# Performance work log

Hardware: AMD Instinct MI355X
Metric: run time of the kernel (lower is better)

Reference implementation:

```python
import jax, jax.numpy as jnp
import numpy as np

EPS = 1e-6
LN3 = 1.0986122886681098  # ternary_softmax uses base-3 exponentials: 3**x / sum(3**x)
ROPE_BASE = 10000.0


def exact_rmsnorm(x, g):
    # ExactRMSNorm: x / sqrt(mean(x^2) + eps) * g
    ms = jnp.mean(jnp.square(x), axis=-1, keepdims=True)
    return x * jax.lax.rsqrt(ms + EPS) * g


def ternary_rope(t):
    # Rotary embedding whose cos/sin tables are quantized to {-1, 0, +1}
    # (round() of cos/sin in [-1,1] yields exactly the ternary set).
    S, D = t.shape[-2], t.shape[-1]
    half = D // 2
    inv_freq = 1.0 / (ROPE_BASE ** (jnp.arange(half, dtype=jnp.float32) / half))
    ang = jnp.arange(S, dtype=jnp.float32)[:, None] * inv_freq[None, :]  # [S, half]
    cos = jnp.round(jnp.cos(ang))
    sin = jnp.round(jnp.sin(ang))
    cos = jnp.concatenate([cos, cos], axis=-1)  # [S, D]
    sin = jnp.concatenate([sin, sin], axis=-1)
    rot = jnp.concatenate([-t[..., half:], t[..., :half]], axis=-1)
    return t * cos + rot * sin


def ternary_softmax(x, axis=-1):
    # softmax in base 3: 3**x / sum(3**x) == softmax(x * ln 3)
    return jax.nn.softmax(x * LN3, axis=axis)


def setup_inputs() -> dict:
    key = jax.random.key(0)
    ks = jax.random.split(key, 6)
    B, S, D = 4, 4096, 1024
    x = jax.random.normal(ks[0], (B, S, D), dtype=jnp.float32)
    g_norm = jnp.ones((D,), dtype=jnp.float32)
    w_qkv = jax.random.normal(ks[1], (D, 3 * D), dtype=jnp.float32) * 0.02
    b_qkv = jnp.zeros((3 * D,), dtype=jnp.float32)
    w_proj = jax.random.normal(ks[2], (D, D), dtype=jnp.float32) * 0.02
    b_proj = jnp.zeros((D,), dtype=jnp.float32)
    return {"x": x, "g_norm": g_norm, "w_qkv": w_qkv, "b_qkv": b_qkv,
            "w_proj": w_proj, "b_proj": b_proj}


def reference(x, g_norm, w_qkv, b_qkv, w_proj, b_proj):
    D = x.shape[-1]
    scale = 1.0 / jnp.sqrt(jnp.float32(D))
    residual = x
    h = exact_rmsnorm(x, g_norm)
    qkv = h @ w_qkv + b_qkv  # [B, S, 3D]
    q, k, v = jnp.split(qkv, 3, axis=-1)
    q = ternary_rope(q)
    k = ternary_rope(k)
    scores = jnp.einsum("bsd,btd->bst", q, k) * scale  # [B, S, S]
    attn = ternary_softmax(scores, axis=-1)
    o = jnp.einsum("bst,btd->bsd", attn, v)
    return o @ w_proj + b_proj + residual
```

## Files before the change

### kernel.cpp

```cpp
#include <hip/hip_runtime.h>
#include <hip/hip_fp8.h>
#include <stdint.h>

#define DEVI __device__ __forceinline__

typedef unsigned short u16;
typedef uint8_t u8;
typedef __attribute__((ext_vector_type(8))) __bf16 bf16x8;
typedef __attribute__((ext_vector_type(4))) float f32x4;
typedef __attribute__((ext_vector_type(4))) int i32x4;
typedef __attribute__((ext_vector_type(8))) int i32x8;

DEVI float b2f(u16 u) { union { unsigned int i; float f; } v; v.i = ((unsigned int)u) << 16; return v.f; }
DEVI u16 f2b(float f) {
  union { float f; unsigned int i; } v; v.f = f;
  unsigned int r = v.i + 0x7fffu + ((v.i >> 16) & 1u);
  return (u16)(r >> 16);
}
DEVI u8 f2f8(float f) { __hip_fp8_e4m3 t(f); return t.__x; }

DEVI void gld_lds16(const void* g, void* l) {
  __builtin_amdgcn_global_load_lds((const __attribute__((address_space(1))) unsigned int*)g,
                                   (__attribute__((address_space(3))) unsigned int*)l, 16, 0, 0);
}

DEVI i32x8 ld32(const u8* p0, const u8* p1) {
  i32x4 lo = *(const i32x4*)p0;
  i32x4 hi = *(const i32x4*)p1;
  return __builtin_shufflevector(lo, hi, 0, 1, 2, 3, 4, 5, 6, 7);
}


__global__ __launch_bounds__(256) void k_rmsnorm(const float* __restrict__ x,
                                                 const float* __restrict__ g,
                                                 u8* __restrict__ h) {
  const int row = blockIdx.x;
  const int t = threadIdx.x;
  const float4 v = ((const float4*)(x + (size_t)row * 1024))[t];
  float ss = v.x * v.x + v.y * v.y + v.z * v.z + v.w * v.w;
  for (int off = 32; off > 0; off >>= 1) ss += __shfl_down(ss, off);
  __shared__ float red[4];
  if ((t & 63) == 0) red[t >> 6] = ss;
  __syncthreads();
  const float tot = red[0] + red[1] + red[2] + red[3];
  const float sc = rsqrtf(tot * (1.0f / 1024.0f) + 1e-6f);
  const float4 gv = ((const float4*)g)[t];
  uchar4 o;
  o.x = f2f8(v.x * sc * gv.x); o.y = f2f8(v.y * sc * gv.y);
  o.z = f2f8(v.z * sc * gv.z); o.w = f2f8(v.w * sc * gv.w);
  *(uchar4*)(h + (size_t)row * 1024 + t * 4) = o;
}

__global__ __launch_bounds__(256) void k_transpose_cast(const float* __restrict__ src,
                                                        int rows, int cols,
                                                        u16* __restrict__ dst) {
  __shared__ float tile[32][33];
  const int c0 = blockIdx.x * 32, r0 = blockIdx.y * 32;
  const int tx = threadIdx.x, ty = threadIdx.y;
  for (int i = 0; i < 32; i += 8)
    tile[ty + i][tx] = src[(size_t)(r0 + ty + i) * cols + c0 + tx];
  __syncthreads();
  for (int i = 0; i < 32; i += 8)
    dst[(size_t)(c0 + ty + i) * rows + r0 + tx] = f2b(tile[tx][ty + i]);
}

__global__ __launch_bounds__(256) void k_transpose_cast_f8(const float* __restrict__ src,
                                                           int rows, int cols,
                                                           u8* __restrict__ dst) {
  __shared__ float tile[32][33];
  const int c0 = blockIdx.x * 32, r0 = blockIdx.y * 32;
  const int tx = threadIdx.x, ty = threadIdx.y;
  for (int i = 0; i < 32; i += 8)
    tile[ty + i][tx] = src[(size_t)(r0 + ty + i) * cols + c0 + tx];
  __syncthreads();
  for (int i = 0; i < 32; i += 8)
    dst[(size_t)(c0 + ty + i) * rows + r0 + tx] = f2f8(tile[tx][ty + i] * 32.0f);
}

__global__ __launch_bounds__(256) void k_rope_cast(const u16* __restrict__ q16, const u16* __restrict__ k16,
                                                   u8* __restrict__ q8, u8* __restrict__ k8) {
  const int row = blockIdx.x;
  const int pos = row & 4095;
  const int t = threadIdx.x;
  const int j0 = t * 2;
  float c[2], s[2];
#pragma unroll
  for (int u = 0; u < 2; u++) {
    const float e = (float)(j0 + u) * (1.0f / 512.0f);
    const float invf = exp2f(-13.287712379549449f * e);
    const float ang = (float)pos * invf;
    c[u] = rintf(cosf(ang));
    s[u] = rintf(sinf(ang));
  }
  const u16* qr = q16 + (size_t)row * 1024;
  const u16* kr = k16 + (size_t)row * 1024;
  u8* qo = q8 + (size_t)row * 1024;
  u8* ko = k8 + (size_t)row * 1024;
  const ushort2 qa = *(const ushort2*)(qr + j0), qb = *(const ushort2*)(qr + j0 + 512);
  const ushort2 ka = *(const ushort2*)(kr + j0), kb = *(const ushort2*)(kr + j0 + 512);
  uchar2 o;
  o.x = f2f8(b2f(qa.x) * c[0] - b2f(qb.x) * s[0]);
  o.y = f2f8(b2f(qa.y) * c[1] - b2f(qb.y) * s[1]);
  *(uchar2*)(qo + j0) = o;
  o.x = f2f8(b2f(qb.x) * c[0] + b2f(qa.x) * s[0]);
  o.y = f2f8(b2f(qb.y) * c[1] + b2f(qa.y) * s[1]);
  *(uchar2*)(qo + j0 + 512) = o;
  o.x = f2f8(b2f(ka.x) * c[0] - b2f(kb.x) * s[0]);
  o.y = f2f8(b2f(ka.y) * c[1] - b2f(kb.y) * s[1]);
  *(uchar2*)(ko + j0) = o;
  o.x = f2f8(b2f(kb.x) * c[0] + b2f(ka.x) * s[0]);
  o.y = f2f8(b2f(kb.y) * c[1] + b2f(ka.y) * s[1]);
  *(uchar2*)(ko + j0 + 512) = o;
}

__global__ __launch_bounds__(256) void k_vt(const u16* __restrict__ v, u8* __restrict__ vt) {
  __shared__ u16 tile[32][33];
  const int b = blockIdx.z;
  const int s0 = blockIdx.x * 32, d0 = blockIdx.y * 32;
  const int tx = threadIdx.x, ty = threadIdx.y;
  for (int i = 0; i < 32; i += 8)
    tile[ty + i][tx] = v[(size_t)(b * 4096 + s0 + ty + i) * 1024 + d0 + tx];
  __syncthreads();
  for (int i = 0; i < 32; i += 8)
    vt[(size_t)(b * 1024 + d0 + ty + i) * 4096 + s0 + tx] = f2f8(b2f(tile[tx][ty + i]));
}

DEVI void gemm_tile(const u16* __restrict__ A, int lda,
                    const u16* __restrict__ B, int ldb,
                    int K, int m0, int n0,
                    u16* As, u16* Bs, f32x4 acc[4][4]) {
  const int t = threadIdx.x;
  const int sr = t >> 2;
  const int sc = (t & 3) * 8;
  const u16* Ag0 = A + (size_t)(m0 + sr) * lda + sc;
  const u16* Ag1 = A + (size_t)(m0 + 64 + sr) * lda + sc;
  const u16* Bg0 = B + (size_t)(n0 + sr) * ldb + sc;
  const u16* Bg1 = B + (size_t)(n0 + 64 + sr) * ldb + sc;
  u16* Asw0 = As + t * 8;
  u16* Asw1 = As + 2048 + t * 8;
  u16* Bsw0 = Bs + t * 8;
  u16* Bsw1 = Bs + 2048 + t * 8;

  const int lane = t & 63, qd = lane >> 4, l16 = lane & 15;
  const int wave = t >> 6;
  const int wm = (wave >> 1) * 64, wn = (wave & 1) * 64;
  const u16* Ard = As + (size_t)(wm + l16) * 32 + qd * 8;
  const u16* Brd = Bs + (size_t)(wn + l16) * 32 + qd * 8;

  for (int k0 = 0; k0 < K; k0 += 32) {
    gld_lds16(Ag0 + k0, Asw0);
    gld_lds16(Ag1 + k0, Asw1);
    gld_lds16(Bg0 + k0, Bsw0);
    gld_lds16(Bg1 + k0, Bsw1);
    __builtin_amdgcn_s_waitcnt(0);
    __syncthreads();
    bf16x8 af[4], bfv[4];
#pragma unroll
    for (int i = 0; i < 4; i++) af[i] = *(const bf16x8*)(Ard + i * 16 * 32);
#pragma unroll
    for (int j = 0; j < 4; j++) bfv[j] = *(const bf16x8*)(Brd + j * 16 * 32);
#pragma unroll
    for (int i = 0; i < 4; i++)
#pragma unroll
      for (int j = 0; j < 4; j++)
        acc[i][j] = __builtin_amdgcn_mfma_f32_16x16x32_bf16(af[i], bfv[j], acc[i][j], 0, 0, 0);
    __syncthreads();
  }
}

DEVI void gemm_tile_mx(const u8* __restrict__ A, int lda,
                       const u8* __restrict__ B, int ldb,
                       int K, int m0, int n0,
                       u8* As, u8* Bs, f32x4 acc[4][4], int sB) {
  const int t = threadIdx.x;
  const int sr = t >> 3;
  const int sc = ((t & 7) ^ (sr & 7)) << 4;
  const u8* Agb = A + (size_t)(m0 + sr) * lda + sc;
  const u8* Bgb = B + (size_t)(n0 + sr) * ldb + sc;
  u8* Asw = As + t * 16;
  u8* Bsw = Bs + t * 16;

  const int lane = t & 63, qd = lane >> 4, l16 = lane & 15;
  const int wave = t >> 6;
  const int wm = (wave >> 1) * 64, wn = (wave & 1) * 64;
  const int key = l16 & 7;
  const int c0 = ((qd << 1) ^ key) << 4;
  const u8* Ar0 = As + (size_t)(wm + l16) * 128 + c0;
  const u8* Ar1 = As + (size_t)(wm + l16) * 128 + (c0 ^ 16);
  const u8* Br0 = Bs + (size_t)(wn + l16) * 128 + c0;
  const u8* Br1 = Bs + (size_t)(wn + l16) * 128 + (c0 ^ 16);

  for (int k0 = 0; k0 < K; k0 += 128) {
#pragma unroll
    for (int l = 0; l < 4; l++) {
      gld_lds16(Agb + k0 + (size_t)l * 32 * lda, Asw + l * 4096);
      gld_lds16(Bgb + k0 + (size_t)l * 32 * ldb, Bsw + l * 4096);
    }
    __builtin_amdgcn_s_waitcnt(0);
    __syncthreads();
    i32x8 a[4], b[4];
#pragma unroll
    for (int i = 0; i < 4; i++) a[i] = ld32(Ar0 + i * 2048, Ar1 + i * 2048);
#pragma unroll
    for (int j = 0; j < 4; j++) b[j] = ld32(Br0 + j * 2048, Br1 + j * 2048);
#pragma unroll
    for (int i = 0; i < 4; i++)
#pragma unroll
      for (int j = 0; j < 4; j++)
        acc[i][j] = __builtin_amdgcn_mfma_scale_f32_16x16x128_f8f6f4(
            a[i], b[j], acc[i][j], 0 , 0 ,
            0, 0x7f7f7f7f, 0, sB);
    __syncthreads();
  }
}

#define ACC_INIT()                                               \
  f32x4 acc[4][4];                                               \
  _Pragma("unroll") for (int i = 0; i < 4; i++)                  \
      _Pragma("unroll") for (int j = 0; j < 4; j++)              \
          acc[i][j] = f32x4{0.f, 0.f, 0.f, 0.f};

#define GEMM_EPI_IDX()                                           \
  const int t = threadIdx.x, lane = t & 63, qd = lane >> 4,      \
            l16 = lane & 15, wave = t >> 6;                      \
  const int wm = (wave >> 1) * 64, wn = (wave & 1) * 64;         \
  (void)t;


__global__ __launch_bounds__(256) void k_gemm_qkv(const u8* __restrict__ A, const u8* __restrict__ Bt,
                                                  const float* __restrict__ bias,
                                                  u16* __restrict__ q16, u16* __restrict__ k16,
                                                  u16* __restrict__ v16) {
  __shared__ alignas(16) u8 As[16384], Bs[16384];
  ACC_INIT();
  const int m0 = blockIdx.y * 128, n0 = blockIdx.x * 128;
  gemm_tile_mx(A, 1024, Bt, 1024, 1024, m0, n0, As, Bs, acc, 0x7a7a7a7a);
  GEMM_EPI_IDX();
  const int sec = n0 >> 10;
  u16* dst = (sec == 0) ? q16 : (sec == 1) ? k16 : v16;
  const int nb0 = n0 & 1023;
#pragma unroll
  for (int i = 0; i < 4; i++) {
    const int mb = m0 + wm + i * 16 + qd * 4;
#pragma unroll
    for (int j = 0; j < 4; j++) {
      const int col = n0 + wn + j * 16 + l16;
      const float bv = bias[col];
      const int dcol = nb0 + wn + j * 16 + l16;
#pragma unroll
      for (int r = 0; r < 4; r++)
        dst[(size_t)(mb + r) * 1024 + dcol] = f2b(acc[i][j][r] + bv);
    }
  }
}

__global__ __launch_bounds__(256) void k_gemm_scores(const u8* __restrict__ q, const u8* __restrict__ kk,
                                                     u8* __restrict__ P, float* __restrict__ ls) {
  __shared__ alignas(16) u8 As[16384], Bs[16384];
  ACC_INIT();
  const int b = blockIdx.z;
  const u8* A = q + (size_t)b * 4096 * 1024;
  const u8* Bt = kk + (size_t)b * 4096 * 1024;
  const int bid = blockIdx.y * 32 + blockIdx.x;
  const int xcd = bid & 7, idx = bid >> 3;
  const int m0 = ((xcd >> 2) * 16 + (idx & 15)) * 128;
  const int n0 = ((xcd & 3) * 8 + (idx >> 4)) * 128;
  gemm_tile_mx(A, 1024, Bt, 1024, 1024, m0, n0, As, Bs, acc, 0x7f7f7f7f);
  GEMM_EPI_IDX();
  const float C3 = 0.04953007814753613f;
  const size_t Pb = (size_t)b * 4096 * 4096;
  f32x4 rowp[4];
#pragma unroll
  for (int i = 0; i < 4; i++) rowp[i] = f32x4{0.f, 0.f, 0.f, 0.f};
#pragma unroll
  for (int i = 0; i < 4; i++) {
    const int mb = m0 + wm + i * 16 + qd * 4;
#pragma unroll
    for (int j = 0; j < 4; j++) {
      const int col = n0 + wn + j * 16 + l16;
#pragma unroll
      for (int r = 0; r < 4; r++) {
        const float pv = exp2f(acc[i][j][r] * C3);
        P[Pb + (size_t)(mb + r) * 4096 + col] = f2f8(pv);
        rowp[i][r] += pv;
      }
    }
  }
#pragma unroll
  for (int m = 1; m < 16; m <<= 1)
#pragma unroll
    for (int i = 0; i < 4; i++) {
      rowp[i].x += __shfl_xor(rowp[i].x, m);
      rowp[i].y += __shfl_xor(rowp[i].y, m);
      rowp[i].z += __shfl_xor(rowp[i].z, m);
      rowp[i].w += __shfl_xor(rowp[i].w, m);
    }
  if (l16 == 0) {
#pragma unroll
    for (int i = 0; i < 4; i++) {
      const int mb = m0 + wm + i * 16 + qd * 4;
#pragma unroll
      for (int r = 0; r < 4; r++)
        atomicAdd(ls + (size_t)b * 4096 + mb + r, rowp[i][r]);
    }
  }
}

__global__ __launch_bounds__(256) void k_gemm_pv(const u8* __restrict__ P, const u8* __restrict__ vt,
                                                 const float* __restrict__ ls, u16* __restrict__ o) {
  __shared__ alignas(16) u8 As[16384], Bs[16384];
  ACC_INIT();
  const int b = blockIdx.z;
  const u8* A = P + (size_t)b * 4096 * 4096;
  const u8* Bt = vt + (size_t)b * 1024 * 4096;
  const int bid = blockIdx.y * 8 + blockIdx.x;
  const int xcd = bid & 7, idx = bid >> 3;
  const int m0 = ((xcd >> 1) * 8 + (idx & 7)) * 128;
  const int n0 = ((xcd & 1) * 4 + (idx >> 3)) * 128;
  gemm_tile_mx(A, 4096, Bt, 4096, 4096, m0, n0, As, Bs, acc, 0x7f7f7f7f);
  GEMM_EPI_IDX();
#pragma unroll
  for (int i = 0; i < 4; i++) {
    const int mb = m0 + wm + i * 16 + qd * 4;
    f32x4 inv;
#pragma unroll
    for (int r = 0; r < 4; r++) inv[r] = 1.0f / ls[(size_t)b * 4096 + mb + r];
#pragma unroll
    for (int j = 0; j < 4; j++) {
      const int col = n0 + wn + j * 16 + l16;
#pragma unroll
      for (int r = 0; r < 4; r++)
        o[(size_t)(b * 4096 + mb + r) * 1024 + col] = f2b(acc[i][j][r] * inv[r]);
    }
  }
}

__global__ __launch_bounds__(256) void k_gemm_proj(const u16* __restrict__ A, const u16* __restrict__ Bt,
                                                   const float* __restrict__ bias, const float* __restrict__ x,
                                                   float* __restrict__ out) {
  __shared__ alignas(16) u16 As[4096], Bs[4096];
  ACC_INIT();
  const int m0 = blockIdx.y * 128, n0 = blockIdx.x * 128;
  gemm_tile(A, 1024, Bt, 1024, 1024, m0, n0, As, Bs, acc);
  GEMM_EPI_IDX();
#pragma unroll
  for (int i = 0; i < 4; i++) {
    const int mb = m0 + wm + i * 16 + qd * 4;
#pragma unroll
    for (int j = 0; j < 4; j++) {
      const int col = n0 + wn + j * 16 + l16;
      const float bv = bias[col];
#pragma unroll
      for (int r = 0; r < 4; r++) {
        const size_t idxo = (size_t)(mb + r) * 1024 + col;
        out[idxo] = acc[i][j][r] + bv + x[idxo];
      }
    }
  }
}

extern "C" void kernel_launch(void* const* d_in, const int* in_sizes, int n_in,
                              void* d_out, int out_size, void* d_ws, size_t ws_size,
                              hipStream_t stream) {
  const float* x     = (const float*)d_in[0];
  const float* g     = (const float*)d_in[1];
  const float* wqkv  = (const float*)d_in[2];
  const float* bqkv  = (const float*)d_in[3];
  const float* wproj = (const float*)d_in[4];
  const float* bproj = (const float*)d_in[5];
  float* out = (float*)d_out;

  char* wsp = (char*)d_ws;
  size_t off = 0;
  auto take = [&](size_t bytes) -> void* {
    off = (off + 255) & ~(size_t)255;
    void* r = wsp + off;
    off += bytes;
    return r;
  };
  char* hreg = (char*)take(16384ull * 1024 * 2);
  u8*  h8   = (u8*)hreg;
  u16* o16  = (u16*)hreg;
  u8*  wqT8 = (u8*)take(3072ull * 1024);
  u16* wpT  = (u16*)take(1024ull * 1024 * 2);
  u8*  q8   = (u8*)take(16384ull * 1024);
  u8*  k8   = (u8*)take(16384ull * 1024);
  u8*  vt   = (u8*)take(4ull * 1024 * 4096);
  float* ls = (float*)take(16384ull * 4);
  char* scratch = (char*)take(3ull * 16384 * 1024 * 2);
  u16* q16 = (u16*)scratch;
  u16* k16 = (u16*)(scratch + 16384ull * 1024 * 2);
  u16* v16 = (u16*)(scratch + 2ull * 16384 * 1024 * 2);
  u8*  P   = (u8*)scratch;

  k_transpose_cast_f8<<<dim3(3072 / 32, 1024 / 32), dim3(32, 8), 0, stream>>>(wqkv, 1024, 3072, wqT8);
  k_transpose_cast<<<dim3(1024 / 32, 1024 / 32), dim3(32, 8), 0, stream>>>(wproj, 1024, 1024, wpT);
  k_rmsnorm<<<16384, 256, 0, stream>>>(x, g, h8);
  k_gemm_qkv<<<dim3(24, 128), 256, 0, stream>>>(h8, wqT8, bqkv, q16, k16, v16);
  k_rope_cast<<<16384, 256, 0, stream>>>(q16, k16, q8, k8);
  k_vt<<<dim3(128, 32, 4), dim3(32, 8), 0, stream>>>(v16, vt);
  hipMemsetAsync(ls, 0, 16384 * 4, stream);
  k_gemm_scores<<<dim3(32, 32, 4), 256, 0, stream>>>(q8, k8, P, ls);
  k_gemm_pv<<<dim3(8, 32, 4), 256, 0, stream>>>(P, vt, ls, o16);
  k_gemm_proj<<<dim3(8, 128), 256, 0, stream>>>(o16, wpT, bproj, x, out);
}
```

Before: 489.3 us.

## Double-buffer LDS tiles in GEMM mainloops to overlap loads with MFMA

Result: slower. 504.1 us (+3.0%).

```diff
diff --git a/kernel.cpp b/kernel.cpp
--- a/kernel.cpp
+++ b/kernel.cpp
@@ -136,24 +136,36 @@
   const u16* Ag1 = A + (size_t)(m0 + 64 + sr) * lda + sc;
   const u16* Bg0 = B + (size_t)(n0 + sr) * ldb + sc;
   const u16* Bg1 = B + (size_t)(n0 + 64 + sr) * ldb + sc;
-  u16* Asw0 = As + t * 8;
-  u16* Asw1 = As + 2048 + t * 8;
-  u16* Bsw0 = Bs + t * 8;
-  u16* Bsw1 = Bs + 2048 + t * 8;
+  u16* Asw = As + t * 8;
+  u16* Bsw = Bs + t * 8;
 
   const int lane = t & 63, qd = lane >> 4, l16 = lane & 15;
   const int wave = t >> 6;
   const int wm = (wave >> 1) * 64, wn = (wave & 1) * 64;
-  const u16* Ard = As + (size_t)(wm + l16) * 32 + qd * 8;
-  const u16* Brd = Bs + (size_t)(wn + l16) * 32 + qd * 8;
-
+  const int aoff = (wm + l16) * 32 + qd * 8;
+  const int boff = (wn + l16) * 32 + qd * 8;
+
+  auto stage = [&](int sel, int k0) {
+    u16* Ad = Asw + sel * 4096;
+    u16* Bd = Bsw + sel * 4096;
+    gld_lds16(Ag0 + k0, Ad);
+    gld_lds16(Ag1 + k0, Ad + 2048);
+    gld_lds16(Bg0 + k0, Bd);
+    gld_lds16(Bg1 + k0, Bd + 2048);
+  };
+
+  stage(0, 0);
+  int cur = 0;
   for (int k0 = 0; k0 < K; k0 += 32) {
-    gld_lds16(Ag0 + k0, Asw0);
-    gld_lds16(Ag1 + k0, Asw1);
-    gld_lds16(Bg0 + k0, Bsw0);
-    gld_lds16(Bg1 + k0, Bsw1);
-    __builtin_amdgcn_s_waitcnt(0);
-    __syncthreads();
+    if (k0 + 32 < K) {
+      stage(cur ^ 1, k0 + 32);
+      asm volatile("s_waitcnt vmcnt(4)" ::: "memory");
+    } else {
+      asm volatile("s_waitcnt vmcnt(0)" ::: "memory");
+    }
+    __builtin_amdgcn_s_barrier();
+    const u16* Ard = As + cur * 4096 + aoff;
+    const u16* Brd = Bs + cur * 4096 + boff;
     bf16x8 af[4], bfv[4];
 #pragma unroll
     for (int i = 0; i < 4; i++) af[i] = *(const bf16x8*)(Ard + i * 16 * 32);
@@ -164,7 +176,8 @@
 #pragma unroll
       for (int j = 0; j < 4; j++)
         acc[i][j] = __builtin_amdgcn_mfma_f32_16x16x32_bf16(af[i], bfv[j], acc[i][j], 0, 0, 0);
-    __syncthreads();
+    __builtin_amdgcn_s_barrier();
+    cur ^= 1;
   }
 }
 
@@ -185,24 +198,38 @@
   const int wm = (wave >> 1) * 64, wn = (wave & 1) * 64;
   const int key = l16 & 7;
   const int c0 = ((qd << 1) ^ key) << 4;
-  const u8* Ar0 = As + (size_t)(wm + l16) * 128 + c0;
-  const u8* Ar1 = As + (size_t)(wm + l16) * 128 + (c0 ^ 16);
-  const u8* Br0 = Bs + (size_t)(wn + l16) * 128 + c0;
-  const u8* Br1 = Bs + (size_t)(wn + l16) * 128 + (c0 ^ 16);
-
+  const int aoff = (wm + l16) * 128 + c0;
+  const int boff = (wn + l16) * 128 + c0;
+
+  auto stage = [&](int sel, int k0) {
+    u8* Ad = Asw + sel * 16384;
+    u8* Bd = Bsw + sel * 16384;
+#pragma unroll
+    for (int l = 0; l < 4; l++) {
+      gld_lds16(Agb + k0 + (size_t)l * 32 * lda, Ad + l * 4096);
+      gld_lds16(Bgb + k0 + (size_t)l * 32 * ldb, Bd + l * 4096);
+    }
+  };
+
+  stage(0, 0);
+  int cur = 0;
   for (int k0 = 0; k0 < K; k0 += 128) {
-#pragma unroll
-    for (int l = 0; l < 4; l++) {
-      gld_lds16(Agb + k0 + (size_t)l * 32 * lda, Asw + l * 4096);
-      gld_lds16(Bgb + k0 + (size_t)l * 32 * ldb, Bsw + l * 4096);
-    }
-    __builtin_amdgcn_s_waitcnt(0);
-    __syncthreads();
+    if (k0 + 128 < K) {
+      stage(cur ^ 1, k0 + 128);
+      asm volatile("s_waitcnt vmcnt(8)" ::: "memory");
+    } else {
+      asm volatile("s_waitcnt vmcnt(0)" ::: "memory");
+    }
+    __builtin_amdgcn_s_barrier();
+    const u8* Ab = As + cur * 16384;
+    const u8* Bb = Bs + cur * 16384;
     i32x8 a[4], b[4];
 #pragma unroll
-    for (int i = 0; i < 4; i++) a[i] = ld32(Ar0 + i * 2048, Ar1 + i * 2048);
-#pragma unroll
-    for (int j = 0; j < 4; j++) b[j] = ld32(Br0 + j * 2048, Br1 + j * 2048);
+    for (int i = 0; i < 4; i++)
+      a[i] = ld32(Ab + aoff + i * 2048, Ab + (aoff ^ 16) + i * 2048);
+#pragma unroll
+    for (int j = 0; j < 4; j++)
+      b[j] = ld32(Bb + boff + j * 2048, Bb + (boff ^ 16) + j * 2048);
 #pragma unroll
     for (int i = 0; i < 4; i++)
 #pragma unroll
@@ -210,7 +237,8 @@
         acc[i][j] = __builtin_amdgcn_mfma_scale_f32_16x16x128_f8f6f4(
             a[i], b[j], acc[i][j], 0 , 0 ,
             0, 0x7f7f7f7f, 0, sB);
-    __syncthreads();
+    __builtin_amdgcn_s_barrier();
+    cur ^= 1;
   }
 }
 
@@ -231,7 +259,7 @@
                                                   const float* __restrict__ bias,
                                                   u16* __restrict__ q16, u16* __restrict__ k16,
                                                   u16* __restrict__ v16) {
-  __shared__ alignas(16) u8 As[16384], Bs[16384];
+  __shared__ alignas(16) u8 As[32768], Bs[32768];
   ACC_INIT();
   const int m0 = blockIdx.y * 128, n0 = blockIdx.x * 128;
   gemm_tile_mx(A, 1024, Bt, 1024, 1024, m0, n0, As, Bs, acc, 0x7a7a7a7a);
@@ -256,7 +284,7 @@
 
 __global__ __launch_bounds__(256) void k_gemm_scores(const u8* __restrict__ q, const u8* __restrict__ kk,
                                                      u8* __restrict__ P, float* __restrict__ ls) {
-  __shared__ alignas(16) u8 As[16384], Bs[16384];
+  __shared__ alignas(16) u8 As[32768], Bs[32768];
   ACC_INIT();
   const int b = blockIdx.z;
   const u8* A = q + (size_t)b * 4096 * 1024;
@@ -280,7 +308,7 @@
       const int col = n0 + wn + j * 16 + l16;
 #pragma unroll
       for (int r = 0; r < 4; r++) {
-        const float pv = exp2f(acc[i][j][r] * C3);
+        const float pv = __builtin_amdgcn_exp2f(acc[i][j][r] * C3);
         P[Pb + (size_t)(mb + r) * 4096 + col] = f2f8(pv);
         rowp[i][r] += pv;
       }
@@ -308,7 +336,7 @@
 
 __global__ __launch_bounds__(256) void k_gemm_pv(const u8* __restrict__ P, const u8* __restrict__ vt,
                                                  const float* __restrict__ ls, u16* __restrict__ o) {
-  __shared__ alignas(16) u8 As[16384], Bs[16384];
+  __shared__ alignas(16) u8 As[32768], Bs[32768];
   ACC_INIT();
   const int b = blockIdx.z;
   const u8* A = P + (size_t)b * 4096 * 4096;
@@ -338,7 +366,7 @@
 __global__ __launch_bounds__(256) void k_gemm_proj(const u16* __restrict__ A, const u16* __restrict__ Bt,
                                                    const float* __restrict__ bias, const float* __restrict__ x,
                                                    float* __restrict__ out) {
-  __shared__ alignas(16) u16 As[4096], Bs[4096];
+  __shared__ alignas(16) u16 As[8192], Bs[8192];
   ACC_INIT();
   const int m0 = blockIdx.y * 128, n0 = blockIdx.x * 128;
   gemm_tile(A, 1024, Bt, 1024, 1024, m0, n0, As, Bs, acc);
```
